# Performance work log

Hardware: AMD Instinct MI355X
Metric: run time of the kernel (lower is better)

The kernel has to match this reference:

```python
import jax, jax.numpy as jnp
import numpy as np

DT_SCALER = 1.0 / 24.0
EULER_STEPS = 10   # odeint euler, t in [0,1], step_size=0.1
STEP = 0.1


def setup_inputs() -> dict:
    key = jax.random.key(0)
    ks = jax.random.split(key, 10)
    B, T, D, H = 8192, 100, 16, 32
    Hd = min((H + D) * 2, 50)  # 50
    x = jax.random.normal(ks[0], (B, T, D), dtype=jnp.float32)
    dt = jax.random.uniform(ks[1], (B, T, 2), dtype=jnp.float32)
    # dh MLP: Linear(H+D -> Hd), tanh, Linear(Hd -> H), tanh ; init N(0, 0.1), bias 0
    W1 = 0.1 * jax.random.normal(ks[2], (Hd, H + D), dtype=jnp.float32)
    b1 = jnp.zeros((Hd,), jnp.float32)
    W2 = 0.1 * jax.random.normal(ks[3], (H, Hd), dtype=jnp.float32)
    b2 = jnp.zeros((H,), jnp.float32)
    # dy MLP: Linear(H -> 2H), tanh, Linear(2H -> 1)
    W3 = 0.1 * jax.random.normal(ks[4], (2 * H, H), dtype=jnp.float32)
    b3 = jnp.zeros((2 * H,), jnp.float32)
    W4 = 0.1 * jax.random.normal(ks[5], (1, 2 * H), dtype=jnp.float32)
    b4 = jnp.zeros((1,), jnp.float32)
    return {"dt": dt, "x": x, "W1": W1, "b1": b1, "W2": W2, "b2": b2,
            "W3": W3, "b3": b3, "W4": W4, "b4": b4}


def _forward(dt, x, W1, b1, W2, b2, W3, b3, W4, b4):
    B, T, D = x.shape
    H = W2.shape[0]
    dti = (dt[:, :, 1] - dt[:, :, 0])[..., None]  # [B,T,1]
    x_t = jnp.swapaxes(x, 0, 1)      # [T,B,D]
    dt_t = jnp.swapaxes(dti, 0, 1)   # [T,B,1]

    def time_step(h, inp):
        x_i, dt_i = inp              # [B,D], [B,1]
        y = x_i[:, 0:1]              # z0 y-part reset to observation each step
        scale = dt_i * DT_SCALER     # [B,1]

        def euler(carry, _):
            y, h = carry
            dh = jnp.tanh(jnp.tanh(jnp.concatenate([x_i, h], axis=1) @ W1.T + b1) @ W2.T + b2) * scale
            dy = (jnp.tanh(h @ W3.T + b3) @ W4.T + b4) * scale
            return (y + STEP * dy, h + STEP * dh), None

        (y, h), _ = jax.lax.scan(euler, (y, h), None, length=EULER_STEPS)
        return h, y

    h0 = jnp.zeros((B, H), jnp.float32)
    _, mu = jax.lax.scan(time_step, h0, (x_t, dt_t))  # mu: [T,B,1]
    return jnp.swapaxes(mu, 0, 1)                     # [B,T,1]


def reference(dt, x, W1, b1, W2, b2, W3, b3, W4, b4):
    return _forward(dt, x, W1, b1, W2, b2, W3, b3, W4, b4)
```

## Files before the change

kernel.cpp:

```cpp
#include <hip/hip_runtime.h>
#include <stdint.h>

#define T_STEPS 100
#define D_IN 16
#define H_DIM 32
#define HD 50
#define KXH 48
#define EULER 10
#define STEPF 0.1f
#define DT_SCALERF (1.0f/24.0f)
#define TANH_SCALE 2.8853900817779268f

typedef __attribute__((ext_vector_type(8))) short short8;
typedef __attribute__((ext_vector_type(4))) float float4v;
typedef __attribute__((ext_vector_type(4))) uint32_t uint4v;

__device__ __forceinline__ float tanh_pre(float us) {
    float e = __builtin_amdgcn_exp2f(us);
    return 1.0f - 2.0f * __builtin_amdgcn_rcpf(e + 1.0f);
}
__device__ __forceinline__ uint32_t pkbf(float lo, float hi) {
    uint32_t r;
    asm("v_cvt_pk_bf16_f32 %0, %1, %2" : "=v"(r) : "v"(lo), "v"(hi));
    return r;
}
__device__ __forceinline__ short f2bf(float f) {
    uint32_t u = __builtin_bit_cast(uint32_t, f);
    u = u + 0x7fffu + ((u >> 16) & 1u);
    return (short)(u >> 16);
}

__device__ __forceinline__ int zorig(int kk) {
    int f = kk >> 5, q = (kk >> 3) & 3, jj = kk & 7;
    int t = 2 * f + (jj >> 2), r = jj & 3;
    if (t < 3) return t * 16 + q * 4 + r;
    if (r == 0 && q < 2) return 48 + q;
    return -1;
}

__global__ __launch_bounds__(128, 1) void latode_kernel(
    const float* __restrict__ dt, const float* __restrict__ x,
    const float* __restrict__ W1, const float* __restrict__ b1,
    const float* __restrict__ W2, const float* __restrict__ b2,
    const float* __restrict__ W3, const float* __restrict__ b3,
    const float* __restrict__ W4, const float* __restrict__ b4,
    float* __restrict__ out)
{
    const int tid  = threadIdx.x;
    const int wave = tid >> 6;
    const int lane = tid & 63;
    const int n16  = lane & 15;
    const int quad = lane >> 4;
    const int b0   = blockIdx.x * 16;

    __shared__ __align__(16) uint32_t hslot[2][256];

    for (int i = tid; i < 512; i += 128) ((uint32_t*)hslot)[i] = 0;

    const float* xrow = x + (size_t)(b0 + n16) * (T_STEPS * D_IN);
    const float* drow = dt + (size_t)(b0 + n16) * (T_STEPS * 2);

    short8 w1h[4], w1x[4], w2f[2][2];
    short8 w3f[4];
    float4v b3v[4], w4v4[4];

    if (wave == 0) {
#pragma unroll
        for (int t = 0; t < 4; ++t) {
            int kz = 32 * (t >> 1) + 8 * (n16 >> 2) + 4 * (t & 1) + (n16 & 3);
            int of = zorig(kz);
#pragma unroll
            for (int j = 0; j < 8; ++j) {
                int kk = quad * 8 + j;
                float wh = 0.0f, wx = 0.0f;
                if (of >= 0) {
                    wh = W1[of * KXH + 16 + kk];
                    if (kk < 16)       wx = W1[of * KXH + kk];
                    else if (kk == 16) wx = b1[of];
                }
                w1h[t][j] = f2bf(wh * TANH_SCALE);
                w1x[t][j] = f2bf(wx * TANH_SCALE);
            }
        }
#pragma unroll
        for (int t2 = 0; t2 < 2; ++t2) {
            int hrow = 8 * (n16 >> 2) + 4 * t2 + (n16 & 3);
#pragma unroll
            for (int kt = 0; kt < 2; ++kt)
#pragma unroll
            for (int j = 0; j < 8; ++j) {
                int kk = kt * 32 + quad * 8 + j;
                int oz = zorig(kk);
                float w = 0.0f;
                if (oz >= 0)       w = W2[hrow * HD + oz];
                else if (kk == 63) w = b2[hrow];
                w2f[t2][kt][j] = f2bf(w * TANH_SCALE);
            }
        }
    } else {
#pragma unroll
        for (int t = 0; t < 4; ++t) {
            int f = t * 16 + n16;
#pragma unroll
            for (int j = 0; j < 8; ++j)
                w3f[t][j] = f2bf(W3[f * H_DIM + quad * 8 + j] * TANH_SCALE);
#pragma unroll
            for (int r = 0; r < 4; ++r) {
                int fr = t * 16 + quad * 4 + r;
                b3v[t][r]  = b3[fr] * TANH_SCALE;
                w4v4[t][r] = W4[fr];
            }
        }
    }
    const float b4s = b4[0];

    float4v hC0 = {0.f,0.f,0.f,0.f}, hC1 = {0.f,0.f,0.f,0.f};
    short8  hB  = {0,0,0,0,0,0,0,0};
    const uint32_t z1d3 = (quad == 3) ? 0x3f800000u : 0u;
    const float4v zero4 = {0.f,0.f,0.f,0.f};

    float4 xa = {0,0,0,0}, xb = {0,0,0,0};
    float2 dtv = {0.f,0.f};
    float y0 = 0.f;
    if (wave == 0) {
        if (quad < 2) { xa = *(const float4*)(xrow + quad * 8);
                        xb = *(const float4*)(xrow + quad * 8 + 4); }
        dtv = *(const float2*)drow;
    } else {
        dtv = *(const float2*)drow;
        y0  = xrow[0];
    }

    __syncthreads();

#pragma unroll 1
    for (int t = 0; t < T_STEPS; ++t) {
        const float s10 = (dtv.y - dtv.x) * (DT_SCALERF * STEPF);
        const float y0c = y0;
        float psum = 0.f;

        float4v cxa[4];
        if (wave == 0) {
            uint4v xp = {0,0,0,0};
            if (quad < 2) {
                xp[0] = pkbf(xa.x, xa.y); xp[1] = pkbf(xa.z, xa.w);
                xp[2] = pkbf(xb.x, xb.y); xp[3] = pkbf(xb.z, xb.w);
            } else if (quad == 2) {
                xp[0] = 0x00003f80u;
            }
            short8 xB = __builtin_bit_cast(short8, xp);
#pragma unroll
            for (int tt = 0; tt < 4; ++tt)
                cxa[tt] = __builtin_amdgcn_mfma_f32_16x16x32_bf16(w1x[tt], xB, zero4, 0, 0, 0);
        }

        {
            int tn = (t + 1 < T_STEPS) ? t + 1 : (T_STEPS - 1);
            if (wave == 0) {
                if (quad < 2) { xa = *(const float4*)(xrow + tn * D_IN + quad * 8);
                                xb = *(const float4*)(xrow + tn * D_IN + quad * 8 + 4); }
                dtv = *(const float2*)(drow + tn * 2);
            } else {
                dtv = *(const float2*)(drow + tn * 2);
                y0  = xrow[tn * D_IN];
            }
        }

#pragma unroll 2
        for (int e = 0; e < EULER; ++e) {
            if (wave == 0) {
                float4v a0 = __builtin_amdgcn_mfma_f32_16x16x32_bf16(w1h[0], hB, cxa[0], 0, 0, 0);
                float4v a1 = __builtin_amdgcn_mfma_f32_16x16x32_bf16(w1h[1], hB, cxa[1], 0, 0, 0);
                float4v a2 = __builtin_amdgcn_mfma_f32_16x16x32_bf16(w1h[2], hB, cxa[2], 0, 0, 0);
                float4v a3 = __builtin_amdgcn_mfma_f32_16x16x32_bf16(w1h[3], hB, cxa[3], 0, 0, 0);
                uint4v z0, z1;
                z0[0] = pkbf(tanh_pre(a0[0]), tanh_pre(a0[1]));
                z0[1] = pkbf(tanh_pre(a0[2]), tanh_pre(a0[3]));
                z0[2] = pkbf(tanh_pre(a1[0]), tanh_pre(a1[1]));
                z0[3] = pkbf(tanh_pre(a1[2]), tanh_pre(a1[3]));
                z1[0] = pkbf(tanh_pre(a2[0]), tanh_pre(a2[1]));
                z1[1] = pkbf(tanh_pre(a2[2]), tanh_pre(a2[3]));
                z1[2] = pkbf(tanh_pre(a3[0]), 0.0f);
                z1[3] = z1d3;
                short8 zf0 = __builtin_bit_cast(short8, z0);
                short8 zf1 = __builtin_bit_cast(short8, z1);
                float4v u20 = __builtin_amdgcn_mfma_f32_16x16x32_bf16(w2f[0][0], zf0, zero4, 0, 0, 0);
                u20 = __builtin_amdgcn_mfma_f32_16x16x32_bf16(w2f[0][1], zf1, u20, 0, 0, 0);
                float4v u21 = __builtin_amdgcn_mfma_f32_16x16x32_bf16(w2f[1][0], zf0, zero4, 0, 0, 0);
                u21 = __builtin_amdgcn_mfma_f32_16x16x32_bf16(w2f[1][1], zf1, u21, 0, 0, 0);
                hC0[0] += s10 * tanh_pre(u20[0]);
                hC0[1] += s10 * tanh_pre(u20[1]);
                hC0[2] += s10 * tanh_pre(u20[2]);
                hC0[3] += s10 * tanh_pre(u20[3]);
                hC1[0] += s10 * tanh_pre(u21[0]);
                hC1[1] += s10 * tanh_pre(u21[1]);
                hC1[2] += s10 * tanh_pre(u21[2]);
                hC1[3] += s10 * tanh_pre(u21[3]);
                uint4v hp;
                hp[0] = pkbf(hC0[0], hC0[1]); hp[1] = pkbf(hC0[2], hC0[3]);
                hp[2] = pkbf(hC1[0], hC1[1]); hp[3] = pkbf(hC1[2], hC1[3]);
                hB = __builtin_bit_cast(short8, hp);
                *(uint4v*)&hslot[(e + 1) & 1][lane * 4] = hp;
            } else {
                short8 hb = __builtin_bit_cast(short8, *(const uint4v*)&hslot[e & 1][lane * 4]);
                float4v a0 = __builtin_amdgcn_mfma_f32_16x16x32_bf16(w3f[0], hb, b3v[0], 0, 0, 0);
                float4v a1 = __builtin_amdgcn_mfma_f32_16x16x32_bf16(w3f[1], hb, b3v[1], 0, 0, 0);
                float4v a2 = __builtin_amdgcn_mfma_f32_16x16x32_bf16(w3f[2], hb, b3v[2], 0, 0, 0);
                float4v a3 = __builtin_amdgcn_mfma_f32_16x16x32_bf16(w3f[3], hb, b3v[3], 0, 0, 0);
                float p0 = w4v4[0][0]*tanh_pre(a0[0]) + w4v4[0][1]*tanh_pre(a0[1])
                         + w4v4[0][2]*tanh_pre(a0[2]) + w4v4[0][3]*tanh_pre(a0[3]);
                float p1 = w4v4[1][0]*tanh_pre(a1[0]) + w4v4[1][1]*tanh_pre(a1[1])
                         + w4v4[1][2]*tanh_pre(a1[2]) + w4v4[1][3]*tanh_pre(a1[3]);
                float p2 = w4v4[2][0]*tanh_pre(a2[0]) + w4v4[2][1]*tanh_pre(a2[1])
                         + w4v4[2][2]*tanh_pre(a2[2]) + w4v4[2][3]*tanh_pre(a2[3]);
                float p3 = w4v4[3][0]*tanh_pre(a3[0]) + w4v4[3][1]*tanh_pre(a3[1])
                         + w4v4[3][2]*tanh_pre(a3[2]) + w4v4[3][3]*tanh_pre(a3[3]);
                float pacc = (p0 + p1) + (p2 + p3);
                pacc += __shfl_xor(pacc, 16, 64);
                pacc += __shfl_xor(pacc, 32, 64);
                psum += pacc;
            }
            __syncthreads();
        }

        if (wave == 1 && lane < 16) {
            out[(size_t)(b0 + n16) * T_STEPS + t] = y0c + s10 * (psum + (float)EULER * b4s);
        }
    }
}

extern "C" void kernel_launch(void* const* d_in, const int* in_sizes, int n_in,
                              void* d_out, int out_size, void* d_ws, size_t ws_size,
                              hipStream_t stream) {
    const float* dt = (const float*)d_in[0];
    const float* x  = (const float*)d_in[1];
    const float* W1 = (const float*)d_in[2];
    const float* b1 = (const float*)d_in[3];
    const float* W2 = (const float*)d_in[4];
    const float* b2 = (const float*)d_in[5];
    const float* W3 = (const float*)d_in[6];
    const float* b3 = (const float*)d_in[7];
    const float* W4 = (const float*)d_in[8];
    const float* b4 = (const float*)d_in[9];
    float* out = (float*)d_out;

    const int B = 8192;
    dim3 grid(B / 16), block(128);
    latode_kernel<<<grid, block, 0, stream>>>(dt, x, W1, b1, W2, b2, W3, b3, W4, b4, out);
}
```

Before: 803.1 us.

## Process two independent 16-row batch groups per block to interleave dependency chains

Each block now handles 32 batch rows as two independent 16-row groups, with their MFMA/tanh chains interleaved inside every Euler step to hide MFMA and transcendental latency. The grid halves to 256 blocks. The cross-lane shuffle reduction for dy moves out of the Euler loop and runs once per time step, and __syncthreads is replaced by an explicit lgkmcnt wait, s_barrier and sched_barrier. In exchange, register pressure rises and only 256 blocks are launched, which on a 256-CU device leaves one 2-wave block per CU.

```diff
diff --git a/kernel.cpp b/kernel.cpp
--- a/kernel.cpp
+++ b/kernel.cpp
@@ -51,14 +51,16 @@
     const int lane = tid & 63;
     const int n16  = lane & 15;
     const int quad = lane >> 4;
-    const int b0   = blockIdx.x * 16;
-
-    __shared__ __align__(16) uint32_t hslot[2][256];
-
-    for (int i = tid; i < 512; i += 128) ((uint32_t*)hslot)[i] = 0;
-
-    const float* xrow = x + (size_t)(b0 + n16) * (T_STEPS * D_IN);
-    const float* drow = dt + (size_t)(b0 + n16) * (T_STEPS * 2);
+    const int b0   = blockIdx.x * 32;
+
+    __shared__ __align__(16) uint32_t hslot[2][2][256];
+
+    for (int i = tid; i < 1024; i += 128) ((uint32_t*)hslot)[i] = 0;
+
+    const float* xr0 = x + (size_t)(b0 + n16) * (T_STEPS * D_IN);
+    const float* dr0 = dt + (size_t)(b0 + n16) * (T_STEPS * 2);
+    const float* xrow[2] = { xr0, xr0 + 16 * T_STEPS * D_IN };
+    const float* drow[2] = { dr0, dr0 + 16 * T_STEPS * 2 };
 
     short8 w1h[4], w1x[4], w2f[2][2];
     short8 w3f[4];
@@ -114,117 +116,158 @@
     }
     const float b4s = b4[0];
 
-    float4v hC0 = {0.f,0.f,0.f,0.f}, hC1 = {0.f,0.f,0.f,0.f};
-    short8  hB  = {0,0,0,0,0,0,0,0};
+    const float4v zero4 = {0.f,0.f,0.f,0.f};
+    float4v hC0[2], hC1[2];
+    short8  hB[2];
+#pragma unroll
+    for (int g = 0; g < 2; ++g) {
+        hC0[g] = zero4; hC1[g] = zero4;
+        hB[g] = (short8){0,0,0,0,0,0,0,0};
+    }
     const uint32_t z1d3 = (quad == 3) ? 0x3f800000u : 0u;
-    const float4v zero4 = {0.f,0.f,0.f,0.f};
-
-    float4 xa = {0,0,0,0}, xb = {0,0,0,0};
-    float2 dtv = {0.f,0.f};
-    float y0 = 0.f;
+
+    float4 xa[2] = {{0,0,0,0},{0,0,0,0}}, xb[2] = {{0,0,0,0},{0,0,0,0}};
+    float2 dtv[2] = {{0.f,0.f},{0.f,0.f}};
+    float y0[2] = {0.f, 0.f};
     if (wave == 0) {
-        if (quad < 2) { xa = *(const float4*)(xrow + quad * 8);
-                        xb = *(const float4*)(xrow + quad * 8 + 4); }
-        dtv = *(const float2*)drow;
+#pragma unroll
+        for (int g = 0; g < 2; ++g) {
+            if (quad < 2) {
+                xa[g] = *(const float4*)(xrow[g] + quad * 8);
+                xb[g] = *(const float4*)(xrow[g] + quad * 8 + 4);
+            }
+            dtv[g] = *(const float2*)drow[g];
+        }
     } else {
-        dtv = *(const float2*)drow;
-        y0  = xrow[0];
+#pragma unroll
+        for (int g = 0; g < 2; ++g) {
+            dtv[g] = *(const float2*)drow[g];
+            y0[g]  = xrow[g][0];
+        }
     }
 
     __syncthreads();
 
 #pragma unroll 1
     for (int t = 0; t < T_STEPS; ++t) {
-        const float s10 = (dtv.y - dtv.x) * (DT_SCALERF * STEPF);
-        const float y0c = y0;
-        float psum = 0.f;
-
-        float4v cxa[4];
+        float s10[2], y0c[2], psum[2];
+#pragma unroll
+        for (int g = 0; g < 2; ++g) {
+            s10[g]  = (dtv[g].y - dtv[g].x) * (DT_SCALERF * STEPF);
+            y0c[g]  = y0[g];
+            psum[g] = 0.f;
+        }
+
+        float4v cxa[2][4];
         if (wave == 0) {
-            uint4v xp = {0,0,0,0};
-            if (quad < 2) {
-                xp[0] = pkbf(xa.x, xa.y); xp[1] = pkbf(xa.z, xa.w);
-                xp[2] = pkbf(xb.x, xb.y); xp[3] = pkbf(xb.z, xb.w);
-            } else if (quad == 2) {
-                xp[0] = 0x00003f80u;
-            }
-            short8 xB = __builtin_bit_cast(short8, xp);
-#pragma unroll
-            for (int tt = 0; tt < 4; ++tt)
-                cxa[tt] = __builtin_amdgcn_mfma_f32_16x16x32_bf16(w1x[tt], xB, zero4, 0, 0, 0);
+#pragma unroll
+            for (int g = 0; g < 2; ++g) {
+                uint4v xp = {0,0,0,0};
+                if (quad < 2) {
+                    xp[0] = pkbf(xa[g].x, xa[g].y); xp[1] = pkbf(xa[g].z, xa[g].w);
+                    xp[2] = pkbf(xb[g].x, xb[g].y); xp[3] = pkbf(xb[g].z, xb[g].w);
+                } else if (quad == 2) {
+                    xp[0] = 0x00003f80u;
+                }
+                short8 xB = __builtin_bit_cast(short8, xp);
+#pragma unroll
+                for (int tt = 0; tt < 4; ++tt)
+                    cxa[g][tt] = __builtin_amdgcn_mfma_f32_16x16x32_bf16(w1x[tt], xB, zero4, 0, 0, 0);
+            }
         }
 
         {
             int tn = (t + 1 < T_STEPS) ? t + 1 : (T_STEPS - 1);
             if (wave == 0) {
-                if (quad < 2) { xa = *(const float4*)(xrow + tn * D_IN + quad * 8);
-                                xb = *(const float4*)(xrow + tn * D_IN + quad * 8 + 4); }
-                dtv = *(const float2*)(drow + tn * 2);
+#pragma unroll
+                for (int g = 0; g < 2; ++g) {
+                    if (quad < 2) {
+                        xa[g] = *(const float4*)(xrow[g] + tn * D_IN + quad * 8);
+                        xb[g] = *(const float4*)(xrow[g] + tn * D_IN + quad * 8 + 4);
+                    }
+                    dtv[g] = *(const float2*)(drow[g] + tn * 2);
+                }
             } else {
-                dtv = *(const float2*)(drow + tn * 2);
-                y0  = xrow[tn * D_IN];
+#pragma unroll
+                for (int g = 0; g < 2; ++g) {
+                    dtv[g] = *(const float2*)(drow[g] + tn * 2);
+                    y0[g]  = xrow[g][tn * D_IN];
+                }
             }
         }
 
 #pragma unroll 2
         for (int e = 0; e < EULER; ++e) {
             if (wave == 0) {
-                float4v a0 = __builtin_amdgcn_mfma_f32_16x16x32_bf16(w1h[0], hB, cxa[0], 0, 0, 0);
-                float4v a1 = __builtin_amdgcn_mfma_f32_16x16x32_bf16(w1h[1], hB, cxa[1], 0, 0, 0);
-                float4v a2 = __builtin_amdgcn_mfma_f32_16x16x32_bf16(w1h[2], hB, cxa[2], 0, 0, 0);
-                float4v a3 = __builtin_amdgcn_mfma_f32_16x16x32_bf16(w1h[3], hB, cxa[3], 0, 0, 0);
-                uint4v z0, z1;
-                z0[0] = pkbf(tanh_pre(a0[0]), tanh_pre(a0[1]));
-                z0[1] = pkbf(tanh_pre(a0[2]), tanh_pre(a0[3]));
-                z0[2] = pkbf(tanh_pre(a1[0]), tanh_pre(a1[1]));
-                z0[3] = pkbf(tanh_pre(a1[2]), tanh_pre(a1[3]));
-                z1[0] = pkbf(tanh_pre(a2[0]), tanh_pre(a2[1]));
-                z1[1] = pkbf(tanh_pre(a2[2]), tanh_pre(a2[3]));
-                z1[2] = pkbf(tanh_pre(a3[0]), 0.0f);
-                z1[3] = z1d3;
-                short8 zf0 = __builtin_bit_cast(short8, z0);
-                short8 zf1 = __builtin_bit_cast(short8, z1);
-                float4v u20 = __builtin_amdgcn_mfma_f32_16x16x32_bf16(w2f[0][0], zf0, zero4, 0, 0, 0);
-                u20 = __builtin_amdgcn_mfma_f32_16x16x32_bf16(w2f[0][1], zf1, u20, 0, 0, 0);
-                float4v u21 = __builtin_amdgcn_mfma_f32_16x16x32_bf16(w2f[1][0], zf0, zero4, 0, 0, 0);
-                u21 = __builtin_amdgcn_mfma_f32_16x16x32_bf16(w2f[1][1], zf1, u21, 0, 0, 0);
-                hC0[0] += s10 * tanh_pre(u20[0]);
-                hC0[1] += s10 * tanh_pre(u20[1]);
-                hC0[2] += s10 * tanh_pre(u20[2]);
-                hC0[3] += s10 * tanh_pre(u20[3]);
-                hC1[0] += s10 * tanh_pre(u21[0]);
-                hC1[1] += s10 * tanh_pre(u21[1]);
-                hC1[2] += s10 * tanh_pre(u21[2]);
-                hC1[3] += s10 * tanh_pre(u21[3]);
-                uint4v hp;
-                hp[0] = pkbf(hC0[0], hC0[1]); hp[1] = pkbf(hC0[2], hC0[3]);
-                hp[2] = pkbf(hC1[0], hC1[1]); hp[3] = pkbf(hC1[2], hC1[3]);
-                hB = __builtin_bit_cast(short8, hp);
-                *(uint4v*)&hslot[(e + 1) & 1][lane * 4] = hp;
+#pragma unroll
+                for (int g = 0; g < 2; ++g) {
+                    float4v a0 = __builtin_amdgcn_mfma_f32_16x16x32_bf16(w1h[0], hB[g], cxa[g][0], 0, 0, 0);
+                    float4v a1 = __builtin_amdgcn_mfma_f32_16x16x32_bf16(w1h[1], hB[g], cxa[g][1], 0, 0, 0);
+                    float4v a2 = __builtin_amdgcn_mfma_f32_16x16x32_bf16(w1h[2], hB[g], cxa[g][2], 0, 0, 0);
+                    float4v a3 = __builtin_amdgcn_mfma_f32_16x16x32_bf16(w1h[3], hB[g], cxa[g][3], 0, 0, 0);
+                    uint4v z0, z1;
+                    z0[0] = pkbf(tanh_pre(a0[0]), tanh_pre(a0[1]));
+                    z0[1] = pkbf(tanh_pre(a0[2]), tanh_pre(a0[3]));
+                    z0[2] = pkbf(tanh_pre(a1[0]), tanh_pre(a1[1]));
+                    z0[3] = pkbf(tanh_pre(a1[2]), tanh_pre(a1[3]));
+                    z1[0] = pkbf(tanh_pre(a2[0]), tanh_pre(a2[1]));
+                    z1[1] = pkbf(tanh_pre(a2[2]), tanh_pre(a2[3]));
+                    z1[2] = pkbf(tanh_pre(a3[0]), 0.0f);
+                    z1[3] = z1d3;
+                    short8 zf0 = __builtin_bit_cast(short8, z0);
+                    short8 zf1 = __builtin_bit_cast(short8, z1);
+                    float4v u20 = __builtin_amdgcn_mfma_f32_16x16x32_bf16(w2f[0][0], zf0, zero4, 0, 0, 0);
+                    u20 = __builtin_amdgcn_mfma_f32_16x16x32_bf16(w2f[0][1], zf1, u20, 0, 0, 0);
+                    float4v u21 = __builtin_amdgcn_mfma_f32_16x16x32_bf16(w2f[1][0], zf0, zero4, 0, 0, 0);
+                    u21 = __builtin_amdgcn_mfma_f32_16x16x32_bf16(w2f[1][1], zf1, u21, 0, 0, 0);
+                    hC0[g][0] += s10[g] * tanh_pre(u20[0]);
+                    hC0[g][1] += s10[g] * tanh_pre(u20[1]);
+                    hC0[g][2] += s10[g] * tanh_pre(u20[2]);
+                    hC0[g][3] += s10[g] * tanh_pre(u20[3]);
+                    hC1[g][0] += s10[g] * tanh_pre(u21[0]);
+                    hC1[g][1] += s10[g] * tanh_pre(u21[1]);
+                    hC1[g][2] += s10[g] * tanh_pre(u21[2]);
+                    hC1[g][3] += s10[g] * tanh_pre(u21[3]);
+                    uint4v hp;
+                    hp[0] = pkbf(hC0[g][0], hC0[g][1]); hp[1] = pkbf(hC0[g][2], hC0[g][3]);
+                    hp[2] = pkbf(hC1[g][0], hC1[g][1]); hp[3] = pkbf(hC1[g][2], hC1[g][3]);
+                    hB[g] = __builtin_bit_cast(short8, hp);
+                    *(uint4v*)&hslot[(e + 1) & 1][g][lane * 4] = hp;
+                }
             } else {
-                short8 hb = __builtin_bit_cast(short8, *(const uint4v*)&hslot[e & 1][lane * 4]);
-                float4v a0 = __builtin_amdgcn_mfma_f32_16x16x32_bf16(w3f[0], hb, b3v[0], 0, 0, 0);
-                float4v a1 = __builtin_amdgcn_mfma_f32_16x16x32_bf16(w3f[1], hb, b3v[1], 0, 0, 0);
-                float4v a2 = __builtin_amdgcn_mfma_f32_16x16x32_bf16(w3f[2], hb, b3v[2], 0, 0, 0);
-                float4v a3 = __builtin_amdgcn_mfma_f32_16x16x32_bf16(w3f[3], hb, b3v[3], 0, 0, 0);
-                float p0 = w4v4[0][0]*tanh_pre(a0[0]) + w4v4[0][1]*tanh_pre(a0[1])
-                         + w4v4[0][2]*tanh_pre(a0[2]) + w4v4[0][3]*tanh_pre(a0[3]);
-                float p1 = w4v4[1][0]*tanh_pre(a1[0]) + w4v4[1][1]*tanh_pre(a1[1])
-                         + w4v4[1][2]*tanh_pre(a1[2]) + w4v4[1][3]*tanh_pre(a1[3]);
-                float p2 = w4v4[2][0]*tanh_pre(a2[0]) + w4v4[2][1]*tanh_pre(a2[1])
-                         + w4v4[2][2]*tanh_pre(a2[2]) + w4v4[2][3]*tanh_pre(a2[3]);
-                float p3 = w4v4[3][0]*tanh_pre(a3[0]) + w4v4[3][1]*tanh_pre(a3[1])
-                         + w4v4[3][2]*tanh_pre(a3[2]) + w4v4[3][3]*tanh_pre(a3[3]);
-                float pacc = (p0 + p1) + (p2 + p3);
+#pragma unroll
+                for (int g = 0; g < 2; ++g) {
+                    short8 hb = __builtin_bit_cast(short8, *(const uint4v*)&hslot[e & 1][g][lane * 4]);
+                    float4v a0 = __builtin_amdgcn_mfma_f32_16x16x32_bf16(w3f[0], hb, b3v[0], 0, 0, 0);
+                    float4v a1 = __builtin_amdgcn_mfma_f32_16x16x32_bf16(w3f[1], hb, b3v[1], 0, 0, 0);
+                    float4v a2 = __builtin_amdgcn_mfma_f32_16x16x32_bf16(w3f[2], hb, b3v[2], 0, 0, 0);
+                    float4v a3 = __builtin_amdgcn_mfma_f32_16x16x32_bf16(w3f[3], hb, b3v[3], 0, 0, 0);
+                    float p0 = w4v4[0][0]*tanh_pre(a0[0]) + w4v4[0][1]*tanh_pre(a0[1])
+                             + w4v4[0][2]*tanh_pre(a0[2]) + w4v4[0][3]*tanh_pre(a0[3]);
+                    float p1 = w4v4[1][0]*tanh_pre(a1[0]) + w4v4[1][1]*tanh_pre(a1[1])
+                             + w4v4[1][2]*tanh_pre(a1[2]) + w4v4[1][3]*tanh_pre(a1[3]);
+                    float p2 = w4v4[2][0]*tanh_pre(a2[0]) + w4v4[2][1]*tanh_pre(a2[1])
+                             + w4v4[2][2]*tanh_pre(a2[2]) + w4v4[2][3]*tanh_pre(a2[3]);
+                    float p3 = w4v4[3][0]*tanh_pre(a3[0]) + w4v4[3][1]*tanh_pre(a3[1])
+                             + w4v4[3][2]*tanh_pre(a3[2]) + w4v4[3][3]*tanh_pre(a3[3]);
+                    psum[g] += (p0 + p1) + (p2 + p3);
+                }
+            }
+            asm volatile("s_waitcnt lgkmcnt(0)" ::: "memory");
+            __builtin_amdgcn_s_barrier();
+            __builtin_amdgcn_sched_barrier(0);
+        }
+
+        if (wave == 1) {
+#pragma unroll
+            for (int g = 0; g < 2; ++g) {
+                float pacc = psum[g];
                 pacc += __shfl_xor(pacc, 16, 64);
                 pacc += __shfl_xor(pacc, 32, 64);
-                psum += pacc;
-            }
-            __syncthreads();
-        }
-
-        if (wave == 1 && lane < 16) {
-            out[(size_t)(b0 + n16) * T_STEPS + t] = y0c + s10 * (psum + (float)EULER * b4s);
+                if (lane < 16)
+                    out[(size_t)(b0 + g * 16 + n16) * T_STEPS + t] =
+                        y0c[g] + s10[g] * (pacc + (float)EULER * b4s);
+            }
         }
     }
 }
@@ -245,6 +288,6 @@
     float* out = (float*)d_out;
 
     const int B = 8192;
-    dim3 grid(B / 16), block(128);
+    dim3 grid(B / 32), block(128);
     latode_kernel<<<grid, block, 0, stream>>>(dt, x, W1, b1, W2, b2, W3, b3, W4, b4, out);
 }
```

Result: slower. 912.3 us (+13.6%).

## Merge dh and dy waves into one wave, removing LDS exchange and barriers

Applied to the files above, without the earlier changes.

Before, two waves split the work: one computed the dh MLP, the other the dy MLP, and they traded h through LDS with a __syncthreads every Euler step. Now a single 64-lane wave does both, reading the dy MLP input straight from the h register fragment. It also defers the cross-quad shuffle reduction to once per time step instead of once per Euler step. This removes the barrier and LDS round trip per step, but doubles the serial MFMA and tanh work per wave, and each block now holds half as many waves.

```diff
diff --git a/kernel.cpp b/kernel.cpp
--- a/kernel.cpp
+++ b/kernel.cpp
@@ -38,7 +38,7 @@
     return -1;
 }
 
-__global__ __launch_bounds__(128, 1) void latode_kernel(
+__global__ __launch_bounds__(64, 1) void latode_kernel(
     const float* __restrict__ dt, const float* __restrict__ x,
     const float* __restrict__ W1, const float* __restrict__ b1,
     const float* __restrict__ W2, const float* __restrict__ b2,
@@ -46,92 +46,78 @@
     const float* __restrict__ W4, const float* __restrict__ b4,
     float* __restrict__ out)
 {
-    const int tid  = threadIdx.x;
-    const int wave = tid >> 6;
-    const int lane = tid & 63;
+    const int lane = threadIdx.x & 63;
     const int n16  = lane & 15;
     const int quad = lane >> 4;
     const int b0   = blockIdx.x * 16;
 
-    __shared__ __align__(16) uint32_t hslot[2][256];
-
-    for (int i = tid; i < 512; i += 128) ((uint32_t*)hslot)[i] = 0;
-
     const float* xrow = x + (size_t)(b0 + n16) * (T_STEPS * D_IN);
     const float* drow = dt + (size_t)(b0 + n16) * (T_STEPS * 2);
 
-    short8 w1h[4], w1x[4], w2f[2][2];
-    short8 w3f[4];
+    short8 w1h[4], w1x[4], w2f[2][2], w3f[4];
     float4v b3v[4], w4v4[4];
 
-    if (wave == 0) {
-#pragma unroll
-        for (int t = 0; t < 4; ++t) {
-            int kz = 32 * (t >> 1) + 8 * (n16 >> 2) + 4 * (t & 1) + (n16 & 3);
-            int of = zorig(kz);
-#pragma unroll
-            for (int j = 0; j < 8; ++j) {
-                int kk = quad * 8 + j;
-                float wh = 0.0f, wx = 0.0f;
-                if (of >= 0) {
-                    wh = W1[of * KXH + 16 + kk];
-                    if (kk < 16)       wx = W1[of * KXH + kk];
-                    else if (kk == 16) wx = b1[of];
-                }
-                w1h[t][j] = f2bf(wh * TANH_SCALE);
-                w1x[t][j] = f2bf(wx * TANH_SCALE);
+#pragma unroll
+    for (int t = 0; t < 4; ++t) {
+        int kz = 32 * (t >> 1) + 8 * (n16 >> 2) + 4 * (t & 1) + (n16 & 3);
+        int of = zorig(kz);
+#pragma unroll
+        for (int j = 0; j < 8; ++j) {
+            int kk = quad * 8 + j;
+            float wh = 0.0f, wx = 0.0f;
+            if (of >= 0) {
+                wh = W1[of * KXH + 16 + kk];
+                if (kk < 16)       wx = W1[of * KXH + kk];
+                else if (kk == 16) wx = b1[of];
             }
-        }
-#pragma unroll
-        for (int t2 = 0; t2 < 2; ++t2) {
-            int hrow = 8 * (n16 >> 2) + 4 * t2 + (n16 & 3);
-#pragma unroll
-            for (int kt = 0; kt < 2; ++kt)
-#pragma unroll
-            for (int j = 0; j < 8; ++j) {
-                int kk = kt * 32 + quad * 8 + j;
-                int oz = zorig(kk);
-                float w = 0.0f;
-                if (oz >= 0)       w = W2[hrow * HD + oz];
-                else if (kk == 63) w = b2[hrow];
-                w2f[t2][kt][j] = f2bf(w * TANH_SCALE);
-            }
-        }
-    } else {
-#pragma unroll
-        for (int t = 0; t < 4; ++t) {
-            int f = t * 16 + n16;
-#pragma unroll
-            for (int j = 0; j < 8; ++j)
-                w3f[t][j] = f2bf(W3[f * H_DIM + quad * 8 + j] * TANH_SCALE);
-#pragma unroll
-            for (int r = 0; r < 4; ++r) {
-                int fr = t * 16 + quad * 4 + r;
-                b3v[t][r]  = b3[fr] * TANH_SCALE;
-                w4v4[t][r] = W4[fr];
-            }
+            w1h[t][j] = f2bf(wh * TANH_SCALE);
+            w1x[t][j] = f2bf(wx * TANH_SCALE);
+        }
+    }
+#pragma unroll
+    for (int t2 = 0; t2 < 2; ++t2) {
+        int hrow = 8 * (n16 >> 2) + 4 * t2 + (n16 & 3);
+#pragma unroll
+        for (int kt = 0; kt < 2; ++kt)
+#pragma unroll
+        for (int j = 0; j < 8; ++j) {
+            int kk = kt * 32 + quad * 8 + j;
+            int oz = zorig(kk);
+            float w = 0.0f;
+            if (oz >= 0)       w = W2[hrow * HD + oz];
+            else if (kk == 63) w = b2[hrow];
+            w2f[t2][kt][j] = f2bf(w * TANH_SCALE);
+        }
+    }
+#pragma unroll
+    for (int t = 0; t < 4; ++t) {
+        int f = t * 16 + n16;
+#pragma unroll
+        for (int j = 0; j < 8; ++j)
+            w3f[t][j] = f2bf(W3[f * H_DIM + quad * 8 + j] * TANH_SCALE);
+#pragma unroll
+        for (int r = 0; r < 4; ++r) {
+            int fr = t * 16 + quad * 4 + r;
+            b3v[t][r]  = b3[fr] * TANH_SCALE;
+            w4v4[t][r] = W4[fr];
         }
     }
     const float b4s = b4[0];
 
-    float4v hC0 = {0.f,0.f,0.f,0.f}, hC1 = {0.f,0.f,0.f,0.f};
-    short8  hB  = {0,0,0,0,0,0,0,0};
+    const float4v zero4 = {0.f,0.f,0.f,0.f};
+    float4v hC0 = zero4, hC1 = zero4;
+    short8  hB  = (short8){0,0,0,0,0,0,0,0};
     const uint32_t z1d3 = (quad == 3) ? 0x3f800000u : 0u;
-    const float4v zero4 = {0.f,0.f,0.f,0.f};
 
     float4 xa = {0,0,0,0}, xb = {0,0,0,0};
-    float2 dtv = {0.f,0.f};
-    float y0 = 0.f;
-    if (wave == 0) {
-        if (quad < 2) { xa = *(const float4*)(xrow + quad * 8);
-                        xb = *(const float4*)(xrow + quad * 8 + 4); }
-        dtv = *(const float2*)drow;
-    } else {
-        dtv = *(const float2*)drow;
-        y0  = xrow[0];
-    }
-
-    __syncthreads();
+    float2 dtv;
+    float y0;
+    if (quad < 2) {
+        xa = *(const float4*)(xrow + quad * 8);
+        xb = *(const float4*)(xrow + quad * 8 + 4);
+    }
+    dtv = *(const float2*)drow;
+    y0  = xrow[0];
 
 #pragma unroll 1
     for (int t = 0; t < T_STEPS; ++t) {
@@ -140,7 +126,7 @@
         float psum = 0.f;
 
         float4v cxa[4];
-        if (wave == 0) {
+        {
             uint4v xp = {0,0,0,0};
             if (quad < 2) {
                 xp[0] = pkbf(xa.x, xa.y); xp[1] = pkbf(xa.z, xa.w);
@@ -156,76 +142,71 @@
 
         {
             int tn = (t + 1 < T_STEPS) ? t + 1 : (T_STEPS - 1);
-            if (wave == 0) {
-                if (quad < 2) { xa = *(const float4*)(xrow + tn * D_IN + quad * 8);
-                                xb = *(const float4*)(xrow + tn * D_IN + quad * 8 + 4); }
-                dtv = *(const float2*)(drow + tn * 2);
-            } else {
-                dtv = *(const float2*)(drow + tn * 2);
-                y0  = xrow[tn * D_IN];
+            if (quad < 2) {
+                xa = *(const float4*)(xrow + tn * D_IN + quad * 8);
+                xb = *(const float4*)(xrow + tn * D_IN + quad * 8 + 4);
             }
+            dtv = *(const float2*)(drow + tn * 2);
+            y0  = xrow[tn * D_IN];
         }
 
 #pragma unroll 2
         for (int e = 0; e < EULER; ++e) {
-            if (wave == 0) {
-                float4v a0 = __builtin_amdgcn_mfma_f32_16x16x32_bf16(w1h[0], hB, cxa[0], 0, 0, 0);
-                float4v a1 = __builtin_amdgcn_mfma_f32_16x16x32_bf16(w1h[1], hB, cxa[1], 0, 0, 0);
-                float4v a2 = __builtin_amdgcn_mfma_f32_16x16x32_bf16(w1h[2], hB, cxa[2], 0, 0, 0);
-                float4v a3 = __builtin_amdgcn_mfma_f32_16x16x32_bf16(w1h[3], hB, cxa[3], 0, 0, 0);
-                uint4v z0, z1;
-                z0[0] = pkbf(tanh_pre(a0[0]), tanh_pre(a0[1]));
-                z0[1] = pkbf(tanh_pre(a0[2]), tanh_pre(a0[3]));
-                z0[2] = pkbf(tanh_pre(a1[0]), tanh_pre(a1[1]));
-                z0[3] = pkbf(tanh_pre(a1[2]), tanh_pre(a1[3]));
-                z1[0] = pkbf(tanh_pre(a2[0]), tanh_pre(a2[1]));
-                z1[1] = pkbf(tanh_pre(a2[2]), tanh_pre(a2[3]));
-                z1[2] = pkbf(tanh_pre(a3[0]), 0.0f);
-                z1[3] = z1d3;
-                short8 zf0 = __builtin_bit_cast(short8, z0);
-                short8 zf1 = __builtin_bit_cast(short8, z1);
-                float4v u20 = __builtin_amdgcn_mfma_f32_16x16x32_bf16(w2f[0][0], zf0, zero4, 0, 0, 0);
-                u20 = __builtin_amdgcn_mfma_f32_16x16x32_bf16(w2f[0][1], zf1, u20, 0, 0, 0);
-                float4v u21 = __builtin_amdgcn_mfma_f32_16x16x32_bf16(w2f[1][0], zf0, zero4, 0, 0, 0);
-                u21 = __builtin_amdgcn_mfma_f32_16x16x32_bf16(w2f[1][1], zf1, u21, 0, 0, 0);
-                hC0[0] += s10 * tanh_pre(u20[0]);
-                hC0[1] += s10 * tanh_pre(u20[1]);
-                hC0[2] += s10 * tanh_pre(u20[2]);
-                hC0[3] += s10 * tanh_pre(u20[3]);
-                hC1[0] += s10 * tanh_pre(u21[0]);
-                hC1[1] += s10 * tanh_pre(u21[1]);
-                hC1[2] += s10 * tanh_pre(u21[2]);
-                hC1[3] += s10 * tanh_pre(u21[3]);
-                uint4v hp;
-                hp[0] = pkbf(hC0[0], hC0[1]); hp[1] = pkbf(hC0[2], hC0[3]);
-                hp[2] = pkbf(hC1[0], hC1[1]); hp[3] = pkbf(hC1[2], hC1[3]);
-                hB = __builtin_bit_cast(short8, hp);
-                *(uint4v*)&hslot[(e + 1) & 1][lane * 4] = hp;
-            } else {
-                short8 hb = __builtin_bit_cast(short8, *(const uint4v*)&hslot[e & 1][lane * 4]);
-                float4v a0 = __builtin_amdgcn_mfma_f32_16x16x32_bf16(w3f[0], hb, b3v[0], 0, 0, 0);
-                float4v a1 = __builtin_amdgcn_mfma_f32_16x16x32_bf16(w3f[1], hb, b3v[1], 0, 0, 0);
-                float4v a2 = __builtin_amdgcn_mfma_f32_16x16x32_bf16(w3f[2], hb, b3v[2], 0, 0, 0);
-                float4v a3 = __builtin_amdgcn_mfma_f32_16x16x32_bf16(w3f[3], hb, b3v[3], 0, 0, 0);
-                float p0 = w4v4[0][0]*tanh_pre(a0[0]) + w4v4[0][1]*tanh_pre(a0[1])
-                         + w4v4[0][2]*tanh_pre(a0[2]) + w4v4[0][3]*tanh_pre(a0[3]);
-                float p1 = w4v4[1][0]*tanh_pre(a1[0]) + w4v4[1][1]*tanh_pre(a1[1])
-                         + w4v4[1][2]*tanh_pre(a1[2]) + w4v4[1][3]*tanh_pre(a1[3]);
-                float p2 = w4v4[2][0]*tanh_pre(a2[0]) + w4v4[2][1]*tanh_pre(a2[1])
-                         + w4v4[2][2]*tanh_pre(a2[2]) + w4v4[2][3]*tanh_pre(a2[3]);
-                float p3 = w4v4[3][0]*tanh_pre(a3[0]) + w4v4[3][1]*tanh_pre(a3[1])
-                         + w4v4[3][2]*tanh_pre(a3[2]) + w4v4[3][3]*tanh_pre(a3[3]);
-                float pacc = (p0 + p1) + (p2 + p3);
-                pacc += __shfl_xor(pacc, 16, 64);
-                pacc += __shfl_xor(pacc, 32, 64);
-                psum += pacc;
-            }
-            __syncthreads();
-        }
-
-        if (wave == 1 && lane < 16) {
-            out[(size_t)(b0 + n16) * T_STEPS + t] = y0c + s10 * (psum + (float)EULER * b4s);
-        }
+            float4v a0 = __builtin_amdgcn_mfma_f32_16x16x32_bf16(w1h[0], hB, cxa[0], 0, 0, 0);
+            float4v a1 = __builtin_amdgcn_mfma_f32_16x16x32_bf16(w1h[1], hB, cxa[1], 0, 0, 0);
+            float4v a2 = __builtin_amdgcn_mfma_f32_16x16x32_bf16(w1h[2], hB, cxa[2], 0, 0, 0);
+            float4v a3 = __builtin_amdgcn_mfma_f32_16x16x32_bf16(w1h[3], hB, cxa[3], 0, 0, 0);
+            float4v c0 = __builtin_amdgcn_mfma_f32_16x16x32_bf16(w3f[0], hB, b3v[0], 0, 0, 0);
+            float4v c1 = __builtin_amdgcn_mfma_f32_16x16x32_bf16(w3f[1], hB, b3v[1], 0, 0, 0);
+            float4v c2 = __builtin_amdgcn_mfma_f32_16x16x32_bf16(w3f[2], hB, b3v[2], 0, 0, 0);
+            float4v c3 = __builtin_amdgcn_mfma_f32_16x16x32_bf16(w3f[3], hB, b3v[3], 0, 0, 0);
+
+            uint4v z0, z1;
+            z0[0] = pkbf(tanh_pre(a0[0]), tanh_pre(a0[1]));
+            z0[1] = pkbf(tanh_pre(a0[2]), tanh_pre(a0[3]));
+            z0[2] = pkbf(tanh_pre(a1[0]), tanh_pre(a1[1]));
+            z0[3] = pkbf(tanh_pre(a1[2]), tanh_pre(a1[3]));
+            z1[0] = pkbf(tanh_pre(a2[0]), tanh_pre(a2[1]));
+            z1[1] = pkbf(tanh_pre(a2[2]), tanh_pre(a2[3]));
+            z1[2] = pkbf(tanh_pre(a3[0]), 0.0f);
+            z1[3] = z1d3;
+            short8 zf0 = __builtin_bit_cast(short8, z0);
+            short8 zf1 = __builtin_bit_cast(short8, z1);
+
+            float4v u20 = __builtin_amdgcn_mfma_f32_16x16x32_bf16(w2f[0][0], zf0, zero4, 0, 0, 0);
+            u20 = __builtin_amdgcn_mfma_f32_16x16x32_bf16(w2f[0][1], zf1, u20, 0, 0, 0);
+            float4v u21 = __builtin_amdgcn_mfma_f32_16x16x32_bf16(w2f[1][0], zf0, zero4, 0, 0, 0);
+            u21 = __builtin_amdgcn_mfma_f32_16x16x32_bf16(w2f[1][1], zf1, u21, 0, 0, 0);
+
+            float p0 = w4v4[0][0]*tanh_pre(c0[0]) + w4v4[0][1]*tanh_pre(c0[1])
+                     + w4v4[0][2]*tanh_pre(c0[2]) + w4v4[0][3]*tanh_pre(c0[3]);
+            float p1 = w4v4[1][0]*tanh_pre(c1[0]) + w4v4[1][1]*tanh_pre(c1[1])
+                     + w4v4[1][2]*tanh_pre(c1[2]) + w4v4[1][3]*tanh_pre(c1[3]);
+            float p2 = w4v4[2][0]*tanh_pre(c2[0]) + w4v4[2][1]*tanh_pre(c2[1])
+                     + w4v4[2][2]*tanh_pre(c2[2]) + w4v4[2][3]*tanh_pre(c2[3]);
+            float p3 = w4v4[3][0]*tanh_pre(c3[0]) + w4v4[3][1]*tanh_pre(c3[1])
+                     + w4v4[3][2]*tanh_pre(c3[2]) + w4v4[3][3]*tanh_pre(c3[3]);
+            psum += (p0 + p1) + (p2 + p3);
+
+            hC0[0] += s10 * tanh_pre(u20[0]);
+            hC0[1] += s10 * tanh_pre(u20[1]);
+            hC0[2] += s10 * tanh_pre(u20[2]);
+            hC0[3] += s10 * tanh_pre(u20[3]);
+            hC1[0] += s10 * tanh_pre(u21[0]);
+            hC1[1] += s10 * tanh_pre(u21[1]);
+            hC1[2] += s10 * tanh_pre(u21[2]);
+            hC1[3] += s10 * tanh_pre(u21[3]);
+            uint4v hp;
+            hp[0] = pkbf(hC0[0], hC0[1]); hp[1] = pkbf(hC0[2], hC0[3]);
+            hp[2] = pkbf(hC1[0], hC1[1]); hp[3] = pkbf(hC1[2], hC1[3]);
+            hB = __builtin_bit_cast(short8, hp);
+        }
+
+        float pacc = psum;
+        pacc += __shfl_xor(pacc, 16, 64);
+        pacc += __shfl_xor(pacc, 32, 64);
+        if (lane < 16)
+            out[(size_t)(b0 + n16) * T_STEPS + t] = y0c + s10 * (pacc + (float)EULER * b4s);
     }
 }
 
@@ -245,6 +226,6 @@
     float* out = (float*)d_out;
 
     const int B = 8192;
-    dim3 grid(B / 16), block(128);
+    dim3 grid(B / 16), block(64);
     latode_kernel<<<grid, block, 0, stream>>>(dt, x, W1, b1, W2, b2, W3, b3, W4, b4, out);
 }
```

After: 690.7 us. 1.16x faster.
